# Performance work log

Measured on AMD Instinct MI355X. Metric: run time of the kernel, lower is better.

The kernel has to match this reference:

```python
import jax, jax.numpy as jnp
import numpy as np
import math

D_PAIR, D_BIAS, H, DH = 128, 128, 4, 32
B, L = 1, 384


def setup_inputs() -> dict:
    key = jax.random.key(0)
    ks = jax.random.split(key, 12)
    s = 0.02
    return {
        "pair": jax.random.normal(ks[0], (B, L, L, D_PAIR), jnp.float32),
        "bias": jax.random.normal(ks[1], (B, L, L, D_BIAS), jnp.float32),
        "ln_g": jnp.ones((D_PAIR,), jnp.float32),
        "ln_b": jnp.zeros((D_PAIR,), jnp.float32),
        "Wq": jax.random.normal(ks[2], (D_PAIR, H * DH), jnp.float32) * s,
        "Wk": jax.random.normal(ks[3], (D_PAIR, H * DH), jnp.float32) * s,
        "Wv": jax.random.normal(ks[4], (D_PAIR, H * DH), jnp.float32) * s,
        "Wb": jax.random.normal(ks[5], (D_BIAS, H), jnp.float32) * s,
        "Wg": jax.random.normal(ks[6], (D_PAIR, H * DH), jnp.float32) * s,
        "bg": jnp.ones((H * DH,), jnp.float32),
        "Wo": jax.random.normal(ks[7], (H * DH, D_PAIR), jnp.float32) * s,
        "bo": jnp.zeros((D_PAIR,), jnp.float32),
    }


def reference(pair, bias, ln_g, ln_b, Wq, Wk, Wv, Wb, Wg, bg, Wo, bo):
    # is_row=True: attend along the first L axis by permuting (i<->n)
    b_, l_ = pair.shape[:2]
    p = jnp.transpose(pair, (0, 2, 1, 3))  # [B,L,L,Dp]
    # LayerNorm over last dim (eps matches torch default)
    mu = jnp.mean(p, axis=-1, keepdims=True)
    var = jnp.mean(jnp.square(p - mu), axis=-1, keepdims=True)
    p = (p - mu) / jnp.sqrt(var + 1e-5) * ln_g + ln_b

    scaling = 1.0 / math.sqrt(DH)
    q = (p @ Wq).reshape(b_, l_, l_, H, DH) * scaling          # [B,n,i,h,c]
    k = (p @ Wk).reshape(b_, l_, l_, H, DH) / math.sqrt(l_)    # [B,n,j,h,c]
    # tied axial attention logits: sum over the n axis + projected bias
    logits = jnp.einsum("bnihc,bnjhc->bijh", q, k) + bias @ Wb  # [B,L,L,h]
    attn = jax.nn.softmax(logits, axis=-2)                      # softmax over j

    v = (p @ Wv).reshape(b_, l_, l_, H, DH)                     # [B,k,j,h,d]
    g = jax.nn.sigmoid(p @ Wg + bg)                             # [B,L,L,h*d]
    o = jnp.einsum("bijh,bkjhd->bikhd", attn, v).reshape(b_, l_, l_, H * DH)
    out = (g * o) @ Wo + bo                                     # [B,L,L,Dp]
    return jnp.transpose(out, (0, 2, 1, 3))  # undo is_row permute
```

## Files before the change

### kernel.cpp

```cpp
#include <hip/hip_runtime.h>
#include <math.h>

typedef unsigned short us;
typedef unsigned long long u64;
typedef short bf16x8 __attribute__((ext_vector_type(8)));
typedef short bf16x4 __attribute__((ext_vector_type(4)));
typedef float f32x4 __attribute__((ext_vector_type(4)));

#define LQ 384
#define DPAIR 128
#define KDIM 12288

#define WT_OFF   0UL
#define P_OFF    262144UL
#define LOG_OFF  262144UL
#define ATT_OFF  2621440UL
#define Q_OFF    38010880UL
#define K_OFF    75759616UL
#define V_OFF    113508352UL
#define G_OFF    151257088UL

__device__ __forceinline__ us f2bf(float x){
  unsigned u = __builtin_bit_cast(unsigned, x);
  return (us)((u + 0x7FFFu + ((u >> 16) & 1u)) >> 16);
}
__device__ __forceinline__ float bf2f(us b){
  unsigned u = ((unsigned)b) << 16;
  return __builtin_bit_cast(float, u);
}
__device__ __forceinline__ void gl_lds16(const void* g, void* l){
  __builtin_amdgcn_global_load_lds((const __attribute__((address_space(1))) unsigned*)g,
                                   (__attribute__((address_space(3))) unsigned*)l, 16, 0, 0);
}
__device__ __forceinline__ float wsum(float x){
  #pragma unroll
  for (int o = 32; o; o >>= 1) x += __shfl_xor(x, o, 64);
  return x;
}
__device__ __forceinline__ float wmaxr(float x){
  #pragma unroll
  for (int o = 32; o; o >>= 1) x = fmaxf(x, __shfl_xor(x, o, 64));
  return x;
}
__device__ __forceinline__ void stage_pair(const us* __restrict__ Arow, const us* __restrict__ Brow,
                                           size_t strideA, size_t strideB, int koff,
                                           us* ldsA, us* ldsB, int tid)
{
  #pragma unroll
  for (int s = 0; s < 4; ++s) {
    int slot = s * 256 + tid;
    int rrow = slot >> 3, cc = slot & 7;
    int cg = cc ^ (rrow & 7);
    gl_lds16(Arow + (size_t)rrow * strideA + koff + cg * 8, &ldsA[slot * 8]);
    gl_lds16(Brow + (size_t)rrow * strideB + koff + cg * 8, &ldsB[slot * 8]);
  }
}

__global__ __launch_bounds__(256) void k_pack(
    const float* __restrict__ Wq, const float* __restrict__ Wk,
    const float* __restrict__ Wv, const float* __restrict__ Wg,
    const float* __restrict__ Wo, us* __restrict__ wt)
{
  int idx = blockIdx.x * 256 + threadIdx.x;
  int m = idx >> 14, rr = idx & 16383, k = rr >> 7, n = rr & 127;
  const float* W; float s;
  switch (m) {
    case 0: W = Wq; s = 0.17677669529663687f; break;
    case 1: W = Wk; s = 0.05103103630798287f; break;
    case 2: W = Wv; s = 1.f; break;
    case 3: W = Wg; s = 1.f; break;
    default: W = Wo; s = 1.f; break;
  }
  wt[m * 16384 + n * 128 + k] = f2bf(W[k * 128 + n] * s);
}

__global__ __launch_bounds__(256) void k_ln(
    const float* __restrict__ pair, const float* __restrict__ lng,
    const float* __restrict__ lnb, us* __restrict__ P)
{
  const int tid = threadIdx.x, w = tid >> 6, l = tid & 63;
  const int gw = blockIdx.x * 4 + w;
  const int b = gw / 12, a0 = (gw % 12) * 32;
  const float2 lg = ((const float2*)lng)[l];
  const float2 lb = ((const float2*)lnb)[l];
  for (int it = 0; it < 8; ++it) {
    float2 x[4];
    #pragma unroll
    for (int rr = 0; rr < 4; ++rr) {
      int a = a0 + it * 4 + rr;
      x[rr] = ((const float2*)(pair + ((size_t)b * LQ + a) * DPAIR))[l];
    }
    #pragma unroll
    for (int rr = 0; rr < 4; ++rr) {
      int a = a0 + it * 4 + rr;
      float s = wsum(x[rr].x + x[rr].y);
      float q = wsum(x[rr].x * x[rr].x + x[rr].y * x[rr].y);
      float mu = s * (1.f / 128.f);
      float var = q * (1.f / 128.f) - mu * mu;
      float rstd = rsqrtf(var + 1e-5f);
      float y0 = (x[rr].x - mu) * rstd * lg.x + lb.x;
      float y1 = (x[rr].y - mu) * rstd * lg.y + lb.y;
      unsigned pk = (unsigned)f2bf(y0) | ((unsigned)f2bf(y1) << 16);
      ((unsigned*)(P + ((size_t)a * LQ + b) * DPAIR))[l] = pk;
    }
  }
}

__global__ __launch_bounds__(256) void k_qkvg(
    const us* __restrict__ P, const us* __restrict__ wt,
    const float* __restrict__ bg,
    us* __restrict__ Qw, us* __restrict__ Kw, us* __restrict__ Vw, us* __restrict__ Gw)
{
  __shared__ __attribute__((aligned(16))) us lds[17408];
  const int tid = threadIdx.x, w = tid >> 6, l = tid & 63;
  const int bx = blockIdx.x;
  const int xg = bx & 7, idx = bx >> 3;
  const int mtile = xg * 144 + (idx >> 2), type = idx & 3;
  const int a = mtile / 3, b0 = (mtile % 3) * 128;
  const size_t Prow0 = (size_t)a * LQ + b0;
  const us* W = wt + type * 16384;
  us* Abuf = lds;
  us* Bbuf = lds + 8192;
  f32x4 acc[4][4];
  #pragma unroll
  for (int mt = 0; mt < 4; ++mt)
    #pragma unroll
    for (int nt = 0; nt < 4; ++nt) acc[mt][nt] = (f32x4){0.f, 0.f, 0.f, 0.f};
  const int m0 = (w & 1) * 64, n0 = (w >> 1) * 64;
  const int row16 = l & 15, kq = l >> 4;
  #pragma unroll
  for (int ks = 0; ks < 2; ++ks) {
    const int koff = ks * 64;
    #pragma unroll
    for (int s = 0; s < 4; ++s) {
      int slot = (s * 4 + w) * 64 + l;
      int rrow = slot >> 3, cc = slot & 7;
      int cg = cc ^ (rrow & 7);
      gl_lds16(P + (Prow0 + rrow) * DPAIR + koff + cg * 8, &Abuf[slot * 8]);
      gl_lds16(W + rrow * DPAIR + koff + cg * 8, &Bbuf[slot * 8]);
    }
    asm volatile("s_waitcnt vmcnt(0)" ::: "memory");
    __syncthreads();
    #pragma unroll
    for (int kb = 0; kb < 2; ++kb) {
      bf16x8 af[4], bv[4];
      #pragma unroll
      for (int mt = 0; mt < 4; ++mt) {
        int r = m0 + mt * 16 + row16;
        int c = (kb * 4 + kq) ^ (r & 7);
        af[mt] = *(const bf16x8*)&Abuf[r * 64 + c * 8];
      }
      #pragma unroll
      for (int nt = 0; nt < 4; ++nt) {
        int r = n0 + nt * 16 + row16;
        int c = (kb * 4 + kq) ^ (r & 7);
        bv[nt] = *(const bf16x8*)&Bbuf[r * 64 + c * 8];
      }
      #pragma unroll
      for (int mt = 0; mt < 4; ++mt)
        #pragma unroll
        for (int nt = 0; nt < 4; ++nt)
          acc[mt][nt] = __builtin_amdgcn_mfma_f32_16x16x32_bf16(af[mt], bv[nt], acc[mt][nt], 0, 0, 0);
    }
    __syncthreads();
  }

  if (type == 2) {
    us* T = lds;
    #pragma unroll
    for (int nt = 0; nt < 4; ++nt) {
      int col = n0 + nt * 16 + row16;
      #pragma unroll
      for (int mt = 0; mt < 4; ++mt) {
        int rowb = m0 + mt * 16 + kq * 4;
        f32x4 vv = acc[mt][nt];
        *(unsigned*)&T[col * 132 + rowb]     = (unsigned)f2bf(vv[0]) | ((unsigned)f2bf(vv[1]) << 16);
        *(unsigned*)&T[col * 132 + rowb + 2] = (unsigned)f2bf(vv[2]) | ((unsigned)f2bf(vv[3]) << 16);
      }
    }
    __syncthreads();
    #pragma unroll
    for (int it = 0; it < 8; ++it) {
      int slot = tid + 256 * it;
      int d = slot >> 4, jc = slot & 15;
      bf16x4 lo = *(const bf16x4*)&T[d * 132 + jc * 8];
      bf16x4 hi = *(const bf16x4*)&T[d * 132 + jc * 8 + 4];
      bf16x8 val = __builtin_shufflevector(lo, hi, 0, 1, 2, 3, 4, 5, 6, 7);
      int h = d >> 5, dd = d & 31;
      *(bf16x8*)&Vw[((size_t)h * KDIM + a * 32 + dd) * LQ + b0 + jc * 8] = val;
    }
  } else {
    us* Cs = lds;
    #pragma unroll
    for (int nt = 0; nt < 4; ++nt) {
      int col = n0 + nt * 16 + row16;
      float bgv = (type == 3) ? bg[col] : 0.f;
      #pragma unroll
      for (int mt = 0; mt < 4; ++mt) {
        f32x4 vv = acc[mt][nt];
        #pragma unroll
        for (int v4 = 0; v4 < 4; ++v4) {
          float x = vv[v4];
          if (type == 3) {
            float e = __expf(-(x + bgv));
            x = 1.f / (1.f + e);
          }
          Cs[(m0 + mt * 16 + kq * 4 + v4) * 136 + col] = f2bf(x);
        }
      }
    }
    __syncthreads();
    #pragma unroll
    for (int it = 0; it < 8; ++it) {
      int slot = tid + 256 * it;
      int row = slot >> 4, chunk = slot & 15;
      bf16x8 val = *(const bf16x8*)&Cs[row * 136 + chunk * 8];
      if (type == 3) {
        *(bf16x8*)&Gw[((size_t)(a * LQ + b0 + row)) * DPAIR + chunk * 8] = val;
      } else {
        int h = chunk >> 2, c8 = chunk & 3;
        us* dst = (type == 0) ? Qw : Kw;
        *(bf16x8*)&dst[((size_t)(h * LQ + b0 + row)) * KDIM + a * 32 + c8 * 8] = val;
      }
    }
  }
}

__global__ __launch_bounds__(256) void k_biasproj(
    const float* __restrict__ bias, const float* __restrict__ Wb,
    float* __restrict__ logits)
{
  __shared__ float bps[128][5];
  const int tid = threadIdx.x, w = tid >> 6, l = tid & 63;
  const int i = blockIdx.x / 3, j0 = (blockIdx.x % 3) * 128;
  const int g = l >> 4, sl = l & 15;
  const float4* Wb4 = (const float4*)Wb;
  float4 wb[8];
  #pragma unroll
  for (int e = 0; e < 8; ++e) wb[e] = Wb4[sl * 8 + e];
  for (int it = 0; it < 8; ++it) {
    int j = j0 + w * 32 + it * 4 + g;
    const float4* br = (const float4*)(bias + ((size_t)i * LQ + j) * DPAIR);
    float4 xa = br[sl * 2], xb = br[sl * 2 + 1];
    float p0 = 0.f, p1 = 0.f, p2 = 0.f, p3 = 0.f;
    #pragma unroll
    for (int e = 0; e < 4; ++e) {
      float xe = ((const float*)&xa)[e];
      p0 += xe * wb[e].x; p1 += xe * wb[e].y; p2 += xe * wb[e].z; p3 += xe * wb[e].w;
      float xf = ((const float*)&xb)[e];
      p0 += xf * wb[4 + e].x; p1 += xf * wb[4 + e].y; p2 += xf * wb[4 + e].z; p3 += xf * wb[4 + e].w;
    }
    #pragma unroll
    for (int o = 1; o < 16; o <<= 1) {
      p0 += __shfl_xor(p0, o, 64);
      p1 += __shfl_xor(p1, o, 64);
      p2 += __shfl_xor(p2, o, 64);
      p3 += __shfl_xor(p3, o, 64);
    }
    if (sl == 0) {
      int row = w * 32 + it * 4 + g;
      bps[row][0] = p0; bps[row][1] = p1; bps[row][2] = p2; bps[row][3] = p3;
    }
  }
  __syncthreads();
  #pragma unroll
  for (int rep = 0; rep < 2; ++rep) {
    int slot = rep * 256 + tid;
    int h = slot >> 7, jj = slot & 127;
    logits[((size_t)h * LQ + i) * LQ + j0 + jj] = bps[jj][h];
  }
}

__global__ __launch_bounds__(256) void k_logits(
    const us* __restrict__ Qw, const us* __restrict__ Kw, float* __restrict__ logits)
{
  __shared__ __attribute__((aligned(16))) us AB[2][2][8192];
  const int tid = threadIdx.x, w = tid >> 6, l = tid & 63;
  const int bx = blockIdx.x;
  const int xg = bx & 7, yg = bx >> 3;
  const int set = xg * 24 + yg / 3, j0 = (yg % 3) * 128;
  const int h = set / 48, rem = set % 48, i0 = (rem / 16) * 128, ks = rem % 16;
  const us* Ab = Qw + (size_t)h * LQ * KDIM + (size_t)i0 * KDIM;
  const us* Bb = Kw + (size_t)h * LQ * KDIM + (size_t)j0 * KDIM;
  f32x4 acc[4][4];
  #pragma unroll
  for (int mt = 0; mt < 4; ++mt)
    #pragma unroll
    for (int nt = 0; nt < 4; ++nt) acc[mt][nt] = (f32x4){0.f, 0.f, 0.f, 0.f};
  const int m0 = (w & 1) * 64, n0 = (w >> 1) * 64;
  const int row16 = l & 15, kq = l >> 4;
  stage_pair(Ab, Bb, KDIM, KDIM, ks * 768, AB[0][0], AB[0][1], tid);
  for (int kk = 0; kk < 12; ++kk) {
    const int cur = kk & 1;
    if (kk < 11) {
      stage_pair(Ab, Bb, KDIM, KDIM, ks * 768 + (kk + 1) * 64, AB[cur ^ 1][0], AB[cur ^ 1][1], tid);
      asm volatile("s_waitcnt vmcnt(8)" ::: "memory");
    } else {
      asm volatile("s_waitcnt vmcnt(0)" ::: "memory");
    }
    __syncthreads();
    #pragma unroll
    for (int kb = 0; kb < 2; ++kb) {
      bf16x8 af[4], bv[4];
      #pragma unroll
      for (int mt = 0; mt < 4; ++mt) {
        int r = m0 + mt * 16 + row16;
        int c = (kb * 4 + kq) ^ (r & 7);
        af[mt] = *(const bf16x8*)&AB[cur][0][r * 64 + c * 8];
      }
      #pragma unroll
      for (int nt = 0; nt < 4; ++nt) {
        int r = n0 + nt * 16 + row16;
        int c = (kb * 4 + kq) ^ (r & 7);
        bv[nt] = *(const bf16x8*)&AB[cur][1][r * 64 + c * 8];
      }
      #pragma unroll
      for (int mt = 0; mt < 4; ++mt)
        #pragma unroll
        for (int nt = 0; nt < 4; ++nt)
          acc[mt][nt] = __builtin_amdgcn_mfma_f32_16x16x32_bf16(af[mt], bv[nt], acc[mt][nt], 0, 0, 0);
    }
    __syncthreads();
  }
  #pragma unroll
  for (int mt = 0; mt < 4; ++mt)
    #pragma unroll
    for (int nt = 0; nt < 4; ++nt)
      #pragma unroll
      for (int v4 = 0; v4 < 4; ++v4) {
        int i = i0 + m0 + mt * 16 + kq * 4 + v4;
        int j = j0 + n0 + nt * 16 + row16;
        atomicAdd(&logits[((size_t)h * LQ + i) * LQ + j], acc[mt][nt][v4]);
      }
}

__global__ __launch_bounds__(256) void k_softmax(
    const float* __restrict__ logits, us* __restrict__ attn)
{
  const int tid = threadIdx.x, h = tid >> 6, l = tid & 63;
  const int i = blockIdx.x;
  const float* lrow = logits + ((size_t)h * LQ + i) * LQ;
  float x[6];
  #pragma unroll
  for (int s = 0; s < 6; ++s) x[s] = lrow[l + 64 * s];
  float mx = x[0];
  #pragma unroll
  for (int s = 1; s < 6; ++s) mx = fmaxf(mx, x[s]);
  mx = wmaxr(mx);
  float e[6], sum = 0.f;
  #pragma unroll
  for (int s = 0; s < 6; ++s) { e[s] = expf(x[s] - mx); sum += e[s]; }
  sum = wsum(sum);
  float rinv = 1.f / sum;
  #pragma unroll
  for (int s = 0; s < 6; ++s)
    attn[((size_t)h * LQ + i) * LQ + l + 64 * s] = f2bf(e[s] * rinv);
}

__global__ __launch_bounds__(256) void k_ogemm(
    const us* __restrict__ attn, const us* __restrict__ Vw, us* __restrict__ Gw)
{
  __shared__ __attribute__((aligned(16))) us AB[2][2][8192];
  const int tid = threadIdx.x, w = tid >> 6, l = tid & 63;
  const int bx = blockIdx.x;
  const int xg = bx & 7, yg = bx >> 3;
  const int set = xg * 48 + yg / 3, i0 = (yg % 3) * 128;
  const int h = set / 96, n0 = (set % 96) * 128;
  const us* Ab = attn + (size_t)h * LQ * LQ + (size_t)i0 * LQ;
  const us* Bb = Vw + (size_t)h * KDIM * LQ + (size_t)n0 * LQ;
  f32x4 acc[4][4];
  #pragma unroll
  for (int mt = 0; mt < 4; ++mt)
    #pragma unroll
    for (int nt = 0; nt < 4; ++nt) acc[mt][nt] = (f32x4){0.f, 0.f, 0.f, 0.f};
  const int m0 = (w & 1) * 64, n0w = (w >> 1) * 64;
  const int row16 = l & 15, kq = l >> 4;
  stage_pair(Ab, Bb, LQ, LQ, 0, AB[0][0], AB[0][1], tid);
  for (int kk = 0; kk < 6; ++kk) {
    const int cur = kk & 1;
    if (kk < 5) {
      stage_pair(Ab, Bb, LQ, LQ, (kk + 1) * 64, AB[cur ^ 1][0], AB[cur ^ 1][1], tid);
      asm volatile("s_waitcnt vmcnt(8)" ::: "memory");
    } else {
      asm volatile("s_waitcnt vmcnt(0)" ::: "memory");
    }
    __syncthreads();
    #pragma unroll
    for (int kb = 0; kb < 2; ++kb) {
      bf16x8 af[4], bv[4];
      #pragma unroll
      for (int mt = 0; mt < 4; ++mt) {
        int r = m0 + mt * 16 + row16;
        int c = (kb * 4 + kq) ^ (r & 7);
        af[mt] = *(const bf16x8*)&AB[cur][0][r * 64 + c * 8];
      }
      #pragma unroll
      for (int nt = 0; nt < 4; ++nt) {
        int r = n0w + nt * 16 + row16;
        int c = (kb * 4 + kq) ^ (r & 7);
        bv[nt] = *(const bf16x8*)&AB[cur][1][r * 64 + c * 8];
      }
      #pragma unroll
      for (int mt = 0; mt < 4; ++mt)
        #pragma unroll
        for (int nt = 0; nt < 4; ++nt)
          acc[mt][nt] = __builtin_amdgcn_mfma_f32_16x16x32_bf16(af[mt], bv[nt], acc[mt][nt], 0, 0, 0);
    }
    __syncthreads();
  }
  us* C = (us*)AB;
  #pragma unroll
  for (int mt = 0; mt < 4; ++mt)
    #pragma unroll
    for (int nt = 0; nt < 4; ++nt)
      #pragma unroll
      for (int v4 = 0; v4 < 4; ++v4)
        C[(m0 + mt * 16 + kq * 4 + v4) * 128 + n0w + nt * 16 + row16] = f2bf(acc[mt][nt][v4]);
  __syncthreads();
  const int k0 = n0 >> 5;
  #pragma unroll
  for (int it = 0; it < 8; ++it) {
    int slot = tid + 256 * it;
    int xr = slot >> 4, ch = slot & 15;
    bf16x8 ov = *(const bf16x8*)&C[xr * 128 + ch * 8];
    size_t eaddr = ((size_t)(i0 + xr) * LQ + k0 + (ch >> 2)) * DPAIR + h * 32 + (ch & 3) * 8;
    bf16x8 gv = *(const bf16x8*)&Gw[eaddr];
    bf16x8 ev;
    #pragma unroll
    for (int q = 0; q < 8; ++q)
      ev[q] = (short)f2bf(bf2f((us)(unsigned short)ov[q]) * bf2f((us)(unsigned short)gv[q]));
    *(bf16x8*)&Gw[eaddr] = ev;
  }
}

__global__ __launch_bounds__(256) void k_final(
    const us* __restrict__ E, const us* __restrict__ wt,
    const float* __restrict__ bo, float* __restrict__ out)
{
  __shared__ __attribute__((aligned(16))) us A[128 * 128];
  const int tid = threadIdx.x, w = tid >> 6, l = tid & 63;
  const int y = blockIdx.x / 3, x0 = (blockIdx.x % 3) * 128;
  #pragma unroll
  for (int s4 = 0; s4 < 8; ++s4) {
    int slot = s4 * 256 + tid;
    int r = slot >> 4, c = slot & 15;
    int cg = (c & 8) | ((c & 7) ^ (r & 7));
    gl_lds16(E + ((size_t)(x0 + r) * LQ + y) * DPAIR + cg * 8, &A[slot * 8]);
  }
  asm volatile("s_waitcnt vmcnt(0)" ::: "memory");
  __syncthreads();
  const us* W = wt + 4 * 16384;
  const int m0 = (w & 1) * 64, n0w = (w >> 1) * 64;
  const int row16 = l & 15, kq = l >> 4;
  f32x4 acc[4][4];
  #pragma unroll
  for (int mt = 0; mt < 4; ++mt)
    #pragma unroll
    for (int nt = 0; nt < 4; ++nt) acc[mt][nt] = (f32x4){0.f, 0.f, 0.f, 0.f};
  #pragma unroll
  for (int kb = 0; kb < 4; ++kb) {
    bf16x8 af[4], bv[4];
    #pragma unroll
    for (int mt = 0; mt < 4; ++mt) {
      int r = m0 + mt * 16 + row16;
      int c = (kb * 4 + kq);
      int cg = (c & 8) | ((c & 7) ^ (r & 7));
      af[mt] = *(const bf16x8*)&A[r * 128 + cg * 8];
    }
    #pragma unroll
    for (int nt = 0; nt < 4; ++nt)
      bv[nt] = *(const bf16x8*)&W[(n0w + nt * 16 + row16) * 128 + kb * 32 + kq * 8];
    #pragma unroll
    for (int mt = 0; mt < 4; ++mt)
      #pragma unroll
      for (int nt = 0; nt < 4; ++nt)
        acc[mt][nt] = __builtin_amdgcn_mfma_f32_16x16x32_bf16(af[mt], bv[nt], acc[mt][nt], 0, 0, 0);
  }
  #pragma unroll
  for (int nt = 0; nt < 4; ++nt) {
    int n = n0w + nt * 16 + row16;
    float bov = bo[n];
    #pragma unroll
    for (int mt = 0; mt < 4; ++mt)
      #pragma unroll
      for (int v4 = 0; v4 < 4; ++v4) {
        int m = m0 + mt * 16 + kq * 4 + v4;
        out[((size_t)y * LQ + x0 + m) * DPAIR + n] = acc[mt][nt][v4] + bov;
      }
  }
}

extern "C" void kernel_launch(void* const* d_in, const int* in_sizes, int n_in,
                              void* d_out, int out_size, void* d_ws, size_t ws_size,
                              hipStream_t stream)
{
  const float* pair = (const float*)d_in[0];
  const float* bias = (const float*)d_in[1];
  const float* lng  = (const float*)d_in[2];
  const float* lnb  = (const float*)d_in[3];
  const float* Wq   = (const float*)d_in[4];
  const float* Wk   = (const float*)d_in[5];
  const float* Wv   = (const float*)d_in[6];
  const float* Wb   = (const float*)d_in[7];
  const float* Wg   = (const float*)d_in[8];
  const float* bg   = (const float*)d_in[9];
  const float* Wo   = (const float*)d_in[10];
  const float* bo   = (const float*)d_in[11];

  char* ws = (char*)d_ws;
  us* wt     = (us*)(ws + WT_OFF);
  us* P      = (us*)(ws + P_OFF);
  us* Qw     = (us*)(ws + Q_OFF);
  us* Kw     = (us*)(ws + K_OFF);
  us* Vw     = (us*)(ws + V_OFF);
  us* Gw     = (us*)(ws + G_OFF);
  us* attn   = (us*)(ws + ATT_OFF);
  float* logits = (float*)(ws + LOG_OFF);

  k_pack<<<320, 256, 0, stream>>>(Wq, Wk, Wv, Wg, Wo, wt);
  k_ln<<<1152, 256, 0, stream>>>(pair, lng, lnb, P);
  k_qkvg<<<4608, 256, 0, stream>>>(P, wt, bg, Qw, Kw, Vw, Gw);
  k_biasproj<<<1152, 256, 0, stream>>>(bias, Wb, logits);
  k_logits<<<576, 256, 0, stream>>>(Qw, Kw, logits);
  k_softmax<<<384, 256, 0, stream>>>(logits, attn);
  k_ogemm<<<1152, 256, 0, stream>>>(attn, Vw, Gw);
  k_final<<<1152, 256, 0, stream>>>(Gw, wt, bo, (float*)d_out);
}
```

Before: 262.4 us.

## Load full-K A tile once into LDS, stream weights directly from global

The QKVG projection kernel now stages the whole 128x128 bf16 A tile from P into LDS in a single pass with an XOR swizzle, replacing two K-stage iterations that each loaded A and B. The weight fragments are read straight from global memory (likely L2-resident) into registers instead of through LDS. This removes one barrier round-trip and half the LDS traffic, and adds an occupancy hint of 4 blocks per SM. The cost is direct global loads in the MFMA loop, which may expose latency, and register pressure under the tighter launch bound.

```diff
diff --git a/kernel.cpp b/kernel.cpp
--- a/kernel.cpp
+++ b/kernel.cpp
@@ -106,7 +106,7 @@
   }
 }
 
-__global__ __launch_bounds__(256) void k_qkvg(
+__global__ __launch_bounds__(256, 4) void k_qkvg(
     const us* __restrict__ P, const us* __restrict__ wt,
     const float* __restrict__ bg,
     us* __restrict__ Qw, us* __restrict__ Kw, us* __restrict__ Vw, us* __restrict__ Gw)
@@ -119,51 +119,44 @@
   const int a = mtile / 3, b0 = (mtile % 3) * 128;
   const size_t Prow0 = (size_t)a * LQ + b0;
   const us* W = wt + type * 16384;
-  us* Abuf = lds;
-  us* Bbuf = lds + 8192;
-  f32x4 acc[4][4];
-  #pragma unroll
-  for (int mt = 0; mt < 4; ++mt)
-    #pragma unroll
-    for (int nt = 0; nt < 4; ++nt) acc[mt][nt] = (f32x4){0.f, 0.f, 0.f, 0.f};
   const int m0 = (w & 1) * 64, n0 = (w >> 1) * 64;
   const int row16 = l & 15, kq = l >> 4;
-  #pragma unroll
-  for (int ks = 0; ks < 2; ++ks) {
-    const int koff = ks * 64;
-    #pragma unroll
-    for (int s = 0; s < 4; ++s) {
-      int slot = (s * 4 + w) * 64 + l;
-      int rrow = slot >> 3, cc = slot & 7;
-      int cg = cc ^ (rrow & 7);
-      gl_lds16(P + (Prow0 + rrow) * DPAIR + koff + cg * 8, &Abuf[slot * 8]);
-      gl_lds16(W + rrow * DPAIR + koff + cg * 8, &Bbuf[slot * 8]);
-    }
-    asm volatile("s_waitcnt vmcnt(0)" ::: "memory");
-    __syncthreads();
-    #pragma unroll
-    for (int kb = 0; kb < 2; ++kb) {
-      bf16x8 af[4], bv[4];
-      #pragma unroll
-      for (int mt = 0; mt < 4; ++mt) {
-        int r = m0 + mt * 16 + row16;
-        int c = (kb * 4 + kq) ^ (r & 7);
-        af[mt] = *(const bf16x8*)&Abuf[r * 64 + c * 8];
-      }
-      #pragma unroll
-      for (int nt = 0; nt < 4; ++nt) {
-        int r = n0 + nt * 16 + row16;
-        int c = (kb * 4 + kq) ^ (r & 7);
-        bv[nt] = *(const bf16x8*)&Bbuf[r * 64 + c * 8];
-      }
-      #pragma unroll
-      for (int mt = 0; mt < 4; ++mt)
-        #pragma unroll
-        for (int nt = 0; nt < 4; ++nt)
-          acc[mt][nt] = __builtin_amdgcn_mfma_f32_16x16x32_bf16(af[mt], bv[nt], acc[mt][nt], 0, 0, 0);
-    }
-    __syncthreads();
-  }
+
+  #pragma unroll
+  for (int s = 0; s < 8; ++s) {
+    int slot = s * 256 + tid;
+    int r = slot >> 4, c = slot & 15;
+    int cg = (c & 8) | ((c & 7) ^ (r & 7));
+    gl_lds16(P + (Prow0 + r) * DPAIR + cg * 8, &lds[slot * 8]);
+  }
+  f32x4 acc[4][4];
+  #pragma unroll
+  for (int mt = 0; mt < 4; ++mt)
+    #pragma unroll
+    for (int nt = 0; nt < 4; ++nt) acc[mt][nt] = (f32x4){0.f, 0.f, 0.f, 0.f};
+  asm volatile("s_waitcnt vmcnt(0)" ::: "memory");
+  __syncthreads();
+
+  #pragma unroll
+  for (int kb = 0; kb < 4; ++kb) {
+    bf16x8 bv[4], af[4];
+    #pragma unroll
+    for (int nt = 0; nt < 4; ++nt)
+      bv[nt] = *(const bf16x8*)&W[(n0 + nt * 16 + row16) * DPAIR + kb * 32 + kq * 8];
+    #pragma unroll
+    for (int mt = 0; mt < 4; ++mt) {
+      int r = m0 + mt * 16 + row16;
+      int c = kb * 4 + kq;
+      int cg = (c & 8) | ((c & 7) ^ (r & 7));
+      af[mt] = *(const bf16x8*)&lds[r * 128 + cg * 8];
+    }
+    #pragma unroll
+    for (int mt = 0; mt < 4; ++mt)
+      #pragma unroll
+      for (int nt = 0; nt < 4; ++nt)
+        acc[mt][nt] = __builtin_amdgcn_mfma_f32_16x16x32_bf16(af[mt], bv[nt], acc[mt][nt], 0, 0, 0);
+  }
+  __syncthreads();
 
   if (type == 2) {
     us* T = lds;
```

Measured after the change: 264.9 us. No clear change (+0.9%).
